# Optimization experiments

Hardware: AMD Instinct MI355X
Metric: run time of the kernel (lower is better)

## Reference

```python
import jax, jax.numpy as jnp
import numpy as np

D_MODEL = 512
PROJ = 2 * D_MODEL  # 1024
N_STATES = 32
KSIZE = 4
LN_EPS = 1e-3  # keras LayerNormalization default epsilon


def setup_inputs() -> dict:
    key = jax.random.key(0)
    ks = jax.random.split(key, 16)
    B, L = 2, 2048
    s_in = 1.0 / np.sqrt(D_MODEL)
    s_pr = 1.0 / np.sqrt(PROJ)
    x = jax.random.normal(ks[0], (B, L, D_MODEL), dtype=jnp.float32)
    # LayerNorm params
    ln_gamma = jnp.ones((D_MODEL,), jnp.float32)
    ln_beta = jnp.zeros((D_MODEL,), jnp.float32)
    # dense1 / dense2: d_model -> proj
    W1 = jax.random.normal(ks[1], (D_MODEL, PROJ), jnp.float32) * s_in
    b1 = jnp.zeros((PROJ,), jnp.float32)
    W2 = jax.random.normal(ks[2], (D_MODEL, PROJ), jnp.float32) * s_in
    b2 = jnp.zeros((PROJ,), jnp.float32)
    # depthwise causal conv1d: kernel (K, 1, PROJ) in WIO layout, groups=PROJ
    conv_k = jax.random.normal(ks[3], (KSIZE, 1, PROJ), jnp.float32) * 0.5
    conv_b = jnp.zeros((PROJ,), jnp.float32)
    # SSM params
    A_log = jnp.log(jnp.broadcast_to(jnp.arange(1, N_STATES + 1, dtype=jnp.float32), (PROJ, N_STATES)))
    D_skip = jnp.ones((PROJ,), jnp.float32)
    WB = jax.random.normal(ks[4], (PROJ, N_STATES), jnp.float32) * s_pr
    bB = jnp.zeros((N_STATES,), jnp.float32)
    WC = jax.random.normal(ks[5], (PROJ, N_STATES), jnp.float32) * s_pr
    bC = jnp.zeros((N_STATES,), jnp.float32)
    Wd = jax.random.normal(ks[6], (PROJ, PROJ), jnp.float32) * s_pr
    bd = jnp.zeros((PROJ,), jnp.float32)
    # dense3: proj -> d_model
    W3 = jax.random.normal(ks[7], (PROJ, D_MODEL), jnp.float32) * s_pr
    b3 = jnp.zeros((D_MODEL,), jnp.float32)
    return dict(x=x, ln_gamma=ln_gamma, ln_beta=ln_beta, W1=W1, b1=b1, W2=W2, b2=b2,
                conv_k=conv_k, conv_b=conv_b, A_log=A_log, D_skip=D_skip,
                WB=WB, bB=bB, WC=WC, bC=bC, Wd=Wd, bd=bd, W3=W3, b3=b3)


def _layernorm(x, gamma, beta):
    mu = jnp.mean(x, axis=-1, keepdims=True)
    var = jnp.mean(jnp.square(x - mu), axis=-1, keepdims=True)
    return (x - mu) * jax.lax.rsqrt(var + LN_EPS) * gamma + beta


def _causal_dwconv(x, k, b):
    # x: [B,L,C], k: [K,1,C], depthwise causal conv (left-pad K-1)
    y = jax.lax.conv_general_dilated(
        x, k, window_strides=(1,), padding=[(KSIZE - 1, 0)],
        dimension_numbers=('NWC', 'WIO', 'NWC'), feature_group_count=PROJ)
    return y + b


def _selective_scan(u, delta, A, Bm, Cm, D_skip):
    # u, delta: [B,L,D]; A: [D,N]; Bm, Cm: [B,L,N]; D_skip: [D]
    deltaA = jnp.einsum('bld,dn->bldn', delta, A)                 # [B,L,D,N]
    deltaBu = jnp.einsum('bld,bld,bln->bldn', delta, u, Bm)        # [B,L,D,N]
    # shift deltaA left by one along L, zero at the end (pad trick in source)
    shifted = jnp.concatenate([deltaA[:, 1:], jnp.zeros_like(deltaA[:, :1])], axis=1)
    # reversed cumsum along L, then exp
    e = jnp.exp(jnp.flip(jnp.cumsum(jnp.flip(shifted, axis=1), axis=1), axis=1))
    xs = jnp.cumsum(deltaBu * e, axis=1) / (e + 1e-12)
    y = jnp.einsum('bldn,bln->bld', xs, Cm)
    return y + u * D_skip


def reference(x, ln_gamma, ln_beta, W1, b1, W2, b2, conv_k, conv_b,
              A_log, D_skip, WB, bB, WC, bC, Wd, bd, W3, b3):
    h = _layernorm(x, ln_gamma, ln_beta)
    x1 = h @ W1 + b1                      # [B,L,PROJ]
    x1 = _causal_dwconv(x1, conv_k, conv_b)
    x1 = jax.nn.silu(x1)
    A = -jnp.exp(A_log)                    # [PROJ,N]
    Cm = x1 @ WC + bC                      # [B,L,N]
    Bm = x1 @ WB + bB                      # [B,L,N]
    delta = jax.nn.softplus(x1 @ Wd + bd)  # [B,L,PROJ]
    y = _selective_scan(x1, delta, A, Bm, Cm, D_skip)
    x2 = jax.nn.silu(h @ W2 + b2)
    out = (y * x2) @ W3 + b3 + x           # residual; dropout is identity at inference
    return out
```

## Files before the change

### kernel.cpp

```cpp
#include <hip/hip_runtime.h>
#include <stdint.h>

#define L_SEQ 2048
#define BATCH 2
#define DMODEL 512
#define PROJ 1024
#define NST 32
#define NCAT 1152
#define ROWS (BATCH*L_SEQ)
#define THRESH 50.0f

typedef float f32x4 __attribute__((ext_vector_type(4)));
typedef short short8 __attribute__((ext_vector_type(8)));

__device__ inline float bf2f(unsigned short u){ uint32_t x=((uint32_t)u)<<16; float f; __builtin_memcpy(&f,&x,4); return f; }
__device__ inline unsigned short f2bf(float f){ uint32_t x; __builtin_memcpy(&x,&f,4); uint32_t r=x+0x7FFFu+((x>>16)&1u); return (unsigned short)(r>>16); }
__device__ inline float siluf(float x){ return x/(1.f+__expf(-x)); }
__device__ inline float softplusf(float x){ return x>20.f? x : log1pf(__expf(x)); }

#define AS1(p) ((const __attribute__((address_space(1))) void*)(p))
#define AS3(p) ((__attribute__((address_space(3))) void*)(p))

template<int N> __device__ inline void wait_vmcnt(){
  if constexpr (N==0)      asm volatile("s_waitcnt vmcnt(0)" ::: "memory");
  else if constexpr (N==4) asm volatile("s_waitcnt vmcnt(4)" ::: "memory");
  else if constexpr (N==8) asm volatile("s_waitcnt vmcnt(8)" ::: "memory");
  else                     asm volatile("s_waitcnt vmcnt(12)" ::: "memory");
}

__global__ __launch_bounds__(256)
void prep_kernel(const float* __restrict__ W1, const float* __restrict__ b1,
                 const float* __restrict__ W2, const float* __restrict__ b2,
                 const float* __restrict__ Wd, const float* __restrict__ bd,
                 const float* __restrict__ WB, const float* __restrict__ bB,
                 const float* __restrict__ WC, const float* __restrict__ bC,
                 const float* __restrict__ W3,
                 unsigned short* __restrict__ W12t, unsigned short* __restrict__ Wcatt,
                 unsigned short* __restrict__ W3t, float* __restrict__ bias12,
                 float* __restrict__ biascat)
{
  __shared__ float tile[32][33];
  int bid = blockIdx.x;
  int lx = threadIdx.x & 31, ly = threadIdx.x >> 5;
  if (bid < 1024) {
    int kt = bid & 15, nt = bid >> 4;
    int k0 = kt*32, n0 = nt*32;
    const float* S = (n0 < 1024) ? W1 : W2;
    int nc = (n0 < 1024) ? n0 : n0 - 1024;
#pragma unroll
    for (int i=0;i<4;i++)
      tile[ly+i*8][lx] = S[(size_t)(k0+ly+i*8)*1024 + nc + lx];
    __syncthreads();
#pragma unroll
    for (int i=0;i<4;i++)
      W12t[(size_t)(n0+ly+i*8)*512 + k0 + lx] = f2bf(tile[lx][ly+i*8]);
    return;
  }
  if (bid < 2176) {
    int t = bid - 1024;
    int kt = t & 31, nt = t >> 5;
    int k0 = kt*32, n0 = nt*32;
#pragma unroll
    for (int i=0;i<4;i++){
      int k = k0 + ly + i*8;
      float v;
      if (n0 < 1024)       v = Wd[(size_t)k*1024 + n0 + lx];
      else if (n0 == 1024) v = WB[(size_t)k*32 + lx];
      else if (n0 == 1056) v = WC[(size_t)k*32 + lx];
      else                 v = 0.f;
      tile[ly+i*8][lx] = v;
    }
    __syncthreads();
#pragma unroll
    for (int i=0;i<4;i++)
      Wcatt[(size_t)(n0+ly+i*8)*1024 + k0 + lx] = f2bf(tile[lx][ly+i*8]);
    return;
  }
  if (bid < 2688) {
    int t = bid - 2176;
    int kt = t & 31, nt = t >> 5;
    int k0 = kt*32, n0 = nt*32;
#pragma unroll
    for (int i=0;i<4;i++)
      tile[ly+i*8][lx] = W3[(size_t)(k0+ly+i*8)*512 + n0 + lx];
    __syncthreads();
#pragma unroll
    for (int i=0;i<4;i++)
      W3t[(size_t)(n0+ly+i*8)*1024 + k0 + lx] = f2bf(tile[lx][ly+i*8]);
    return;
  }
  int j = (bid - 2688)*256 + threadIdx.x;
  if (j < 2048) { bias12[j] = (j < 1024) ? b1[j] : b2[j-1024]; return; }
  j -= 2048;
  if (j < NCAT) biascat[j] = (j < 1024) ? bd[j] : (j < 1056) ? bB[j-1024] : (j < 1088) ? bC[j-1056] : 0.f;
}

__global__ __launch_bounds__(256)
void ln_kernel(const float* __restrict__ x, const float* __restrict__ gamma,
               const float* __restrict__ beta, unsigned short* __restrict__ H)
{
  int row = blockIdx.x*4 + (threadIdx.x >> 6);
  int lane = threadIdx.x & 63;
  const float4* xr = (const float4*)(x + (size_t)row*DMODEL);
  float4 v0 = xr[lane];
  float4 v1 = xr[lane+64];
  float s = v0.x+v0.y+v0.z+v0.w + v1.x+v1.y+v1.z+v1.w;
  float q = v0.x*v0.x+v0.y*v0.y+v0.z*v0.z+v0.w*v0.w
          + v1.x*v1.x+v1.y*v1.y+v1.z*v1.z+v1.w*v1.w;
#pragma unroll
  for (int m=32;m>0;m>>=1){ s += __shfl_xor(s,m); q += __shfl_xor(q,m); }
  float mu = s*(1.f/DMODEL);
  float var = q*(1.f/DMODEL) - mu*mu;
  float rs = rsqrtf(var + 1e-3f);
  int c0 = lane*4, c1 = 256 + lane*4;
  float4 g0 = *(const float4*)&gamma[c0]; float4 g1 = *(const float4*)&gamma[c1];
  float4 t0 = *(const float4*)&beta[c0];  float4 t1 = *(const float4*)&beta[c1];
  ushort4 o0, o1;
  o0.x = f2bf((v0.x-mu)*rs*g0.x + t0.x);
  o0.y = f2bf((v0.y-mu)*rs*g0.y + t0.y);
  o0.z = f2bf((v0.z-mu)*rs*g0.z + t0.z);
  o0.w = f2bf((v0.w-mu)*rs*g0.w + t0.w);
  o1.x = f2bf((v1.x-mu)*rs*g1.x + t1.x);
  o1.y = f2bf((v1.y-mu)*rs*g1.y + t1.y);
  o1.z = f2bf((v1.z-mu)*rs*g1.z + t1.z);
  o1.w = f2bf((v1.w-mu)*rs*g1.w + t1.w);
  *(ushort4*)&H[(size_t)row*DMODEL + c0] = o0;
  *(ushort4*)&H[(size_t)row*DMODEL + c1] = o1;
}

template<int MODE>
__global__ __launch_bounds__(256)
void gemm128(const unsigned short* __restrict__ A, const unsigned short* __restrict__ Bt,
             void* __restrict__ Cv, const float* __restrict__ bias,
             int M, int N, int K)
{
  constexpr int BK = 64;
  constexpr int LPT = 8;
  __shared__ unsigned short As[2][128*BK];
  __shared__ unsigned short Bs[2][128*BK];
  int tid = threadIdx.x;
  int lane = tid & 63, wid = tid >> 6;
  int wm = wid >> 1, wn = wid & 1;

  int gx = gridDim.x;
  int nwg = gx * gridDim.y;
  int L = blockIdx.y*gx + blockIdx.x;
  int W = (L & 7)*(nwg >> 3) + (L >> 3);
  int bx = W % gx, by = W / gx;
  int m0 = bx*128, n0 = by*128;

  f32x4 acc[4][4];
#pragma unroll
  for (int i=0;i<4;i++)
#pragma unroll
    for (int j=0;j<4;j++)
#pragma unroll
      for (int e=0;e<4;e++) acc[i][j][e] = 0.f;

  const unsigned short* ap[4];
  const unsigned short* bp[4];
#pragma unroll
  for (int j=0;j<4;j++){
    int s = tid + j*256;
    int row = s >> 3, kc = ((s & 7) ^ (row & 7)) * 8;
    ap[j] = A + (size_t)(m0+row)*K + kc;
    bp[j] = Bt + (size_t)(n0+row)*K + kc;
  }

  auto stage = [&](int buf){
#pragma unroll
    for (int j=0;j<4;j++){
      __builtin_amdgcn_global_load_lds(AS1(ap[j]), AS3(&As[buf][(size_t)(j*256 + wid*64)*8]), 16, 0, 0);
      ap[j] += BK;
    }
#pragma unroll
    for (int j=0;j<4;j++){
      __builtin_amdgcn_global_load_lds(AS1(bp[j]), AS3(&Bs[buf][(size_t)(j*256 + wid*64)*8]), 16, 0, 0);
      bp[j] += BK;
    }
  };

  stage(0);
  stage(1);
  int T = K/BK;
  int r = lane & 15, kb = lane >> 4;
  for (int t = 0; t < T; ++t) {
    int rb = t & 1;
    if (t+1 < T) wait_vmcnt<LPT>();
    else         wait_vmcnt<0>();
    __builtin_amdgcn_s_barrier();
    short8 af[2][4], bfr[2][4];
#pragma unroll
    for (int ks=0; ks<2; ++ks) {
      int cx = (ks*4 + kb) ^ (r & 7);
#pragma unroll
      for (int i=0;i<4;i++){
        int row = wm*64 + i*16 + r;
        af[ks][i] = *(const short8*)&As[rb][(row*8 + cx)*8];
      }
#pragma unroll
      for (int j=0;j<4;j++){
        int row = wn*64 + j*16 + r;
        bfr[ks][j] = *(const short8*)&Bs[rb][(row*8 + cx)*8];
      }
    }
    asm volatile("s_waitcnt lgkmcnt(0)" ::: "memory");
    __builtin_amdgcn_sched_barrier(0);
    __builtin_amdgcn_s_barrier();
    if (t+2 < T) stage(rb);
    __builtin_amdgcn_s_setprio(1);
#pragma unroll
    for (int ks=0; ks<2; ++ks)
#pragma unroll
      for (int i=0;i<4;i++)
#pragma unroll
        for (int j=0;j<4;j++)
          acc[i][j] = __builtin_amdgcn_mfma_f32_16x16x32_bf16(af[ks][i], bfr[ks][j], acc[i][j], 0,0,0);
    __builtin_amdgcn_s_setprio(0);
  }

  int rr = (lane >> 4)*4, cc = lane & 15;
#pragma unroll
  for (int i=0;i<4;i++)
#pragma unroll
    for (int j=0;j<4;j++) {
      int col = n0 + wn*64 + j*16 + cc;
      float bcol = (MODE == 1) ? bias[col] : 0.f;
#pragma unroll
      for (int e=0;e<4;e++) {
        int row = m0 + wm*64 + i*16 + rr + e;
        float v = acc[i][j][e];
        if constexpr (MODE == 2) {
          v += bias[row];
          if (row < 1024) v = softplusf(v);
          ((float*)Cv)[(size_t)row*N + col] = v;
        } else {
          ((unsigned short*)Cv)[(size_t)row*N + col] = f2bf(v + bcol);
        }
      }
    }
}

__global__ __launch_bounds__(256)
void gemm64s(const unsigned short* __restrict__ A, const unsigned short* __restrict__ Bt,
             float* __restrict__ Pp, int M, int N, int K, int Kfull)
{
  constexpr int BK = 64;
  constexpr int LPT = 4;
  __shared__ unsigned short As[3][64*BK];
  __shared__ unsigned short Bs[3][64*BK];
  int tid = threadIdx.x;
  int lane = tid & 63, wid = tid >> 6;
  int wm = wid >> 1, wn = wid & 1;
  int gx = gridDim.x;
  int nwg = gx * gridDim.y;
  int L = blockIdx.y*gx + blockIdx.x;
  int W = (L & 7)*(nwg >> 3) + (L >> 3);
  int bx = W % gx, by = W / gx;
  int m0 = bx*64, n0 = by*64;
  int kofs = blockIdx.z*K;

  f32x4 acc[2][2];
#pragma unroll
  for (int i=0;i<2;i++)
#pragma unroll
    for (int j=0;j<2;j++)
#pragma unroll
      for (int e=0;e<4;e++) acc[i][j][e] = 0.f;

  const unsigned short* ap[2];
  const unsigned short* bp[2];
#pragma unroll
  for (int j=0;j<2;j++){
    int s = tid + j*256;
    int row = s >> 3, kc = ((s & 7) ^ (row & 7)) * 8;
    ap[j] = A + (size_t)(m0+row)*Kfull + kofs + kc;
    bp[j] = Bt + (size_t)(n0+row)*Kfull + kofs + kc;
  }
  auto stage = [&](int buf){
#pragma unroll
    for (int j=0;j<2;j++){
      __builtin_amdgcn_global_load_lds(AS1(ap[j]), AS3(&As[buf][(size_t)(j*256 + wid*64)*8]), 16, 0, 0);
      ap[j] += BK;
    }
#pragma unroll
    for (int j=0;j<2;j++){
      __builtin_amdgcn_global_load_lds(AS1(bp[j]), AS3(&Bs[buf][(size_t)(j*256 + wid*64)*8]), 16, 0, 0);
      bp[j] += BK;
    }
  };
  stage(0); stage(1);
  int T = K/BK;
  int rb = 0, wb = 2;
  int r = lane & 15, kb = lane >> 4;
  for (int t = 0; t < T; ++t) {
    if (t+1 < T) wait_vmcnt<LPT>();
    else         wait_vmcnt<0>();
    __builtin_amdgcn_s_barrier();
    if (t+2 < T) { stage(wb); wb = (wb==2)?0:wb+1; }
#pragma unroll
    for (int ks=0; ks<2; ++ks) {
      int cx = (ks*4 + kb) ^ (r & 7);
      short8 af[2], bfr[2];
#pragma unroll
      for (int i=0;i<2;i++) af[i]  = *(const short8*)&As[rb][((wm*32 + i*16 + r)*8 + cx)*8];
#pragma unroll
      for (int j=0;j<2;j++) bfr[j] = *(const short8*)&Bs[rb][((wn*32 + j*16 + r)*8 + cx)*8];
      __builtin_amdgcn_s_setprio(1);
#pragma unroll
      for (int i=0;i<2;i++)
#pragma unroll
        for (int j=0;j<2;j++)
          acc[i][j] = __builtin_amdgcn_mfma_f32_16x16x32_bf16(af[i], bfr[j], acc[i][j], 0,0,0);
      __builtin_amdgcn_s_setprio(0);
    }
    rb = (rb==2)?0:rb+1;
  }
  int rr = (lane >> 4)*4, cc = lane & 15;
#pragma unroll
  for (int i=0;i<2;i++)
#pragma unroll
    for (int j=0;j<2;j++) {
      int col = n0 + wn*32 + j*16 + cc;
#pragma unroll
      for (int e=0;e<4;e++) {
        int row = m0 + wm*32 + i*16 + rr + e;
        Pp[(size_t)blockIdx.z*M*N + (size_t)row*N + col] = acc[i][j][e];
      }
    }
}

__global__ __launch_bounds__(256)
void reduce_kernel(const float* __restrict__ P, const float* __restrict__ x,
                   const float* __restrict__ b3, float* __restrict__ out)
{
  size_t i = ((size_t)blockIdx.x*256 + threadIdx.x)*4;
  int col = (int)(i & 511);
  float4 a = *(const float4*)&P[i];
  float4 b = *(const float4*)&P[(size_t)ROWS*512 + i];
  float4 xv = *(const float4*)&x[i];
  float4 bv = *(const float4*)&b3[col];
  float4 o;
  o.x = a.x + b.x + xv.x + bv.x;
  o.y = a.y + b.y + xv.y + bv.y;
  o.z = a.z + b.z + xv.z + bv.z;
  o.w = a.w + b.w + xv.w + bv.w;
  *(float4*)&out[i] = o;
}

__global__ __launch_bounds__(256)
void conv_silu_kernel(const unsigned short* __restrict__ P12, const float* __restrict__ ck,
                      const float* __restrict__ cb, unsigned short* __restrict__ ubf,
                      unsigned short* __restrict__ x2bf)
{
  int gid = blockIdx.x*256 + threadIdx.x;
  int c4 = gid & 511;
  int row = gid >> 9;
  int l = row & (L_SEQ-1);
  if (c4 < 256) {
    int c = c4*4;
    float4 bv = *(const float4*)&cb[c];
    float r0=bv.x, r1=bv.y, r2=bv.z, r3=bv.w;
#pragma unroll
    for (int t=0;t<4;t++){
      int lsrc = l - 3 + t;
      if (lsrc >= 0) {
        ushort4 xv = *(const ushort4*)&P12[(size_t)(row-3+t)*2048 + c];
        float4 kv = *(const float4*)&ck[t*PROJ + c];
        r0 = fmaf(bf2f(xv.x),kv.x,r0);
        r1 = fmaf(bf2f(xv.y),kv.y,r1);
        r2 = fmaf(bf2f(xv.z),kv.z,r2);
        r3 = fmaf(bf2f(xv.w),kv.w,r3);
      }
    }
    ushort4 o;
    o.x=f2bf(siluf(r0)); o.y=f2bf(siluf(r1)); o.z=f2bf(siluf(r2)); o.w=f2bf(siluf(r3));
    *(ushort4*)&ubf[(size_t)row*PROJ + c] = o;
  } else {
    int c = (c4-256)*4;
    ushort4 xv = *(const ushort4*)&P12[(size_t)row*2048 + 1024 + c];
    ushort4 o;
    o.x=f2bf(siluf(bf2f(xv.x))); o.y=f2bf(siluf(bf2f(xv.y)));
    o.z=f2bf(siluf(bf2f(xv.z))); o.w=f2bf(siluf(bf2f(xv.w)));
    *(ushort4*)&x2bf[(size_t)row*PROJ + c] = o;
  }
}

__global__ __launch_bounds__(256)
void sscan_kernel(const float* __restrict__ CT, const unsigned short* __restrict__ ubf,
                  const float* __restrict__ A_log, int* __restrict__ l0out,
                  unsigned short* __restrict__ ystate)
{
  __shared__ float suf8sh[8][256];
  int tid = threadIdx.x;
  int n = tid & 31, gsub = tid >> 5;
  int G = blockIdx.x*8 + gsub;
  int b = G >> 10, d = G & 1023;
  const float* dT = CT + (size_t)d*ROWS + b*L_SEQ;

  float mysum = 0.f;
  {
    const float4* c4 = (const float4*)(dT + n*64);
    for (int it=0; it<16; ++it){ float4 v = c4[it]; mysum += v.x+v.y+v.z+v.w; }
  }
  float incl = mysum;
#pragma unroll
  for (int dlt=1; dlt<32; dlt<<=1){ float t = __shfl_up(incl, dlt, 32); if (n >= dlt) incl += t; }
  float Tot = __shfl(incl, 31, 32);
  float excl = incl - mysum;
  int cnt = 0;
  {
    const float4* c4 = (const float4*)(dT + n*64);
    float run = excl;
    for (int it=0; it<16; ++it){
      float4 v = c4[it];
      if ((it & 1) == 0) suf8sh[gsub][n*8 + (it>>1)] = Tot - run;
      cnt += (Tot - run >= THRESH); run += v.x;
      cnt += (Tot - run >= THRESH); run += v.y;
      cnt += (Tot - run >= THRESH); run += v.z;
      cnt += (Tot - run >= THRESH); run += v.w;
    }
  }
#pragma unroll
  for (int m=16;m>0;m>>=1) cnt += __shfl_xor(cnt, m, 32);
  int myl0 = cnt > 0 ? cnt-1 : 0;
  if (n == 0) l0out[G] = myl0;
  __syncthreads();

  int base = min(myl0, __shfl_xor(myl0, 32)) & ~7;
  float np1 = __expf(A_log[d*NST + n]);
  const float* Br = CT + (size_t)(1024+n)*ROWS + b*L_SEQ;
  const float* Cr = CT + (size_t)(1056+n)*ROWS + b*L_SEQ;
  const unsigned short* ub = ubf + (size_t)b*L_SEQ*PROJ + d;
  unsigned short* yb = ystate + (size_t)b*L_SEQ*PROJ + d;
  float s = 0.f;
  for (int l = base; l < L_SEQ; l += 8) {
    float4 d0 = *(const float4*)&dT[l];
    float4 d1 = *(const float4*)&dT[l+4];
    float4 B0 = *(const float4*)&Br[l];
    float4 B1 = *(const float4*)&Br[l+4];
    float4 C0 = *(const float4*)&Cr[l];
    float4 C1 = *(const float4*)&Cr[l+4];
    float sufv = suf8sh[gsub][l >> 3];
    float dl[8] = {d0.x,d0.y,d0.z,d0.w,d1.x,d1.y,d1.z,d1.w};
    float Bv[8] = {B0.x,B0.y,B0.z,B0.w,B1.x,B1.y,B1.z,B1.w};
    float Cv[8] = {C0.x,C0.y,C0.z,C0.w,C1.x,C1.y,C1.z,C1.w};
    float uu[8];
#pragma unroll
    for (int t=0;t<8;t++) uu[t] = bf2f(ub[(size_t)(l+t)*PROJ]);
    float cum = 0.f;
#pragma unroll
    for (int t=0;t<8;t++){
      cum += dl[t];
      float decay = __expf(-dl[t]*np1);
      s = fmaf(decay, s, dl[t]*uu[t]*Bv[t]);
      float gte = 1.f/(1.f + 1e-12f*__expf(np1*(sufv - cum)));
      float contrib = s*gte*Cv[t];
#pragma unroll
      for (int m=16;m>0;m>>=1) contrib += __shfl_xor(contrib, m);
      if (n == 0) yb[(size_t)(l+t)*PROJ] = f2bf(contrib);
    }
  }
}

__global__ __launch_bounds__(256)
void zmul_kernel(const unsigned short* __restrict__ ystate, const unsigned short* __restrict__ ubf,
                 const unsigned short* __restrict__ x2bf, const float* __restrict__ Dskip,
                 const int* __restrict__ l0arr, unsigned short* __restrict__ zbf)
{
  size_t i = ((size_t)blockIdx.x*256 + threadIdx.x)*4;
  int d = (int)(i & (PROJ-1));
  int row = (int)(i >> 10);
  int l = row & (L_SEQ-1);
  int b = row >> 11;
  int4 l0v = *(const int4*)&l0arr[b*PROJ + d];
  ushort4 yu = *(const ushort4*)&ystate[i];
  float ysx = (l >= l0v.x) ? bf2f(yu.x) : 0.f;
  float ysy = (l >= l0v.y) ? bf2f(yu.y) : 0.f;
  float ysz = (l >= l0v.z) ? bf2f(yu.z) : 0.f;
  float ysw = (l >= l0v.w) ? bf2f(yu.w) : 0.f;
  ushort4 uu = *(const ushort4*)&ubf[i];
  ushort4 xx = *(const ushort4*)&x2bf[i];
  float4 Dv = *(const float4*)&Dskip[d];
  ushort4 o;
  o.x = f2bf((ysx + bf2f(uu.x)*Dv.x)*bf2f(xx.x));
  o.y = f2bf((ysy + bf2f(uu.y)*Dv.y)*bf2f(xx.y));
  o.z = f2bf((ysz + bf2f(uu.z)*Dv.z)*bf2f(xx.z));
  o.w = f2bf((ysw + bf2f(uu.w)*Dv.w)*bf2f(xx.w));
  *(ushort4*)&zbf[i] = o;
}

extern "C" void kernel_launch(void* const* d_in, const int* in_sizes, int n_in,
                              void* d_out, int out_size, void* d_ws, size_t ws_size,
                              hipStream_t stream)
{
  const float* x     = (const float*)d_in[0];
  const float* ln_g  = (const float*)d_in[1];
  const float* ln_b  = (const float*)d_in[2];
  const float* W1    = (const float*)d_in[3];
  const float* b1    = (const float*)d_in[4];
  const float* W2    = (const float*)d_in[5];
  const float* b2    = (const float*)d_in[6];
  const float* convk = (const float*)d_in[7];
  const float* convb = (const float*)d_in[8];
  const float* A_log = (const float*)d_in[9];
  const float* Dskip = (const float*)d_in[10];
  const float* WB    = (const float*)d_in[11];
  const float* bB    = (const float*)d_in[12];
  const float* WC    = (const float*)d_in[13];
  const float* bC    = (const float*)d_in[14];
  const float* Wd    = (const float*)d_in[15];
  const float* bd    = (const float*)d_in[16];
  const float* W3    = (const float*)d_in[17];
  const float* b3    = (const float*)d_in[18];

  char* w = (char*)d_ws;
  auto alloc = [&](size_t bytes){ char* p = w; w += (bytes + 255) & ~(size_t)255; return p; };
  unsigned short* Hbf    = (unsigned short*)alloc((size_t)ROWS*DMODEL*2);
  unsigned short* W12t   = (unsigned short*)alloc((size_t)2048*512*2);
  unsigned short* Wcatt  = (unsigned short*)alloc((size_t)NCAT*1024*2);
  unsigned short* W3t    = (unsigned short*)alloc((size_t)512*1024*2);
  float*          bias12 = (float*)alloc(2048*4);
  float*          biascat= (float*)alloc(NCAT*4);
  unsigned short* P12    = (unsigned short*)alloc((size_t)ROWS*2048*2);
  unsigned short* ubf    = (unsigned short*)alloc((size_t)ROWS*PROJ*2);
  unsigned short* x2bf   = (unsigned short*)alloc((size_t)ROWS*PROJ*2);
  float*          CT     = (float*)alloc((size_t)NCAT*ROWS*4);
  int*            l0arr  = (int*)alloc(2048*4);
  unsigned short* ystate = (unsigned short*)alloc((size_t)ROWS*PROJ*2);
  unsigned short* zbf    = (unsigned short*)alloc((size_t)ROWS*PROJ*2);
  float*          Pp     = (float*)alloc((size_t)2*ROWS*512*4);

  prep_kernel<<<2701, 256, 0, stream>>>(W1,b1,W2,b2,Wd,bd,WB,bB,WC,bC,W3,
                                        W12t,Wcatt,W3t,bias12,biascat);
  ln_kernel<<<ROWS/4, 256, 0, stream>>>(x, ln_g, ln_b, Hbf);

  dim3 g1(ROWS/128, 2048/128);
  gemm128<1><<<g1, 256, 0, stream>>>(Hbf, W12t, P12, bias12, ROWS, 2048, DMODEL);

  conv_silu_kernel<<<ROWS*512/256, 256, 0, stream>>>(P12, convk, convb, ubf, x2bf);

  dim3 g2(NCAT/128, ROWS/128);
  gemm128<2><<<g2, 256, 0, stream>>>(Wcatt, ubf, CT, biascat, NCAT, ROWS, PROJ);

  sscan_kernel<<<2048/8, 256, 0, stream>>>(CT, ubf, A_log, l0arr, ystate);

  zmul_kernel<<<(ROWS*PROJ/4)/256, 256, 0, stream>>>(ystate, ubf, x2bf, Dskip, l0arr, zbf);

  dim3 g3(ROWS/64, 512/64, 2);
  gemm64s<<<g3, 256, 0, stream>>>(zbf, W3t, Pp, ROWS, 512, 512, PROJ);
  reduce_kernel<<<(ROWS*512/4)/256, 256, 0, stream>>>(Pp, x, b3, (float*)d_out);
}
```

Measured before the change: 159.8 us.

## Fuse LN into prep, silu x2 into GEMM epilogue, zmul into scan

Merges weight prep and layernorm into one launch and applies silu for x2 directly in the first GEMM epilogue, so conv only handles the u half. It drops the padded 1152 concat to 1088 columns and moves that GEMM to 64-wide tiles. The scan now writes the final z = (y + u*D)*x2 itself, with a pre-pass filling u*D*x2 for positions before each channel's start index. This removes the ystate and l0 buffers and the separate zmul pass. The cost is extra per-element work inside the serial scan and a smaller-tile GEMM that may reuse data less.

```diff
diff --git a/kernel.cpp b/kernel.cpp
--- a/kernel.cpp
+++ b/kernel.cpp
@@ -6,7 +6,7 @@
 #define DMODEL 512
 #define PROJ 1024
 #define NST 32
-#define NCAT 1152
+#define NCATU 1088
 #define ROWS (BATCH*L_SEQ)
 #define THRESH 50.0f
 
@@ -29,15 +29,17 @@
 }
 
 __global__ __launch_bounds__(256)
-void prep_kernel(const float* __restrict__ W1, const float* __restrict__ b1,
-                 const float* __restrict__ W2, const float* __restrict__ b2,
-                 const float* __restrict__ Wd, const float* __restrict__ bd,
-                 const float* __restrict__ WB, const float* __restrict__ bB,
-                 const float* __restrict__ WC, const float* __restrict__ bC,
-                 const float* __restrict__ W3,
-                 unsigned short* __restrict__ W12t, unsigned short* __restrict__ Wcatt,
-                 unsigned short* __restrict__ W3t, float* __restrict__ bias12,
-                 float* __restrict__ biascat)
+void prep_ln_kernel(const float* __restrict__ W1, const float* __restrict__ b1,
+                    const float* __restrict__ W2, const float* __restrict__ b2,
+                    const float* __restrict__ Wd, const float* __restrict__ bd,
+                    const float* __restrict__ WB, const float* __restrict__ bB,
+                    const float* __restrict__ WC, const float* __restrict__ bC,
+                    const float* __restrict__ W3,
+                    unsigned short* __restrict__ W12t, unsigned short* __restrict__ Wcatt,
+                    unsigned short* __restrict__ W3t, float* __restrict__ bias12,
+                    float* __restrict__ biascat,
+                    const float* __restrict__ x, const float* __restrict__ ln_g,
+                    const float* __restrict__ ln_b, unsigned short* __restrict__ H)
 {
   __shared__ float tile[32][33];
   int bid = blockIdx.x;
@@ -56,7 +58,7 @@
       W12t[(size_t)(n0+ly+i*8)*512 + k0 + lx] = f2bf(tile[lx][ly+i*8]);
     return;
   }
-  if (bid < 2176) {
+  if (bid < 2112) {
     int t = bid - 1024;
     int kt = t & 31, nt = t >> 5;
     int k0 = kt*32, n0 = nt*32;
@@ -66,8 +68,7 @@
       float v;
       if (n0 < 1024)       v = Wd[(size_t)k*1024 + n0 + lx];
       else if (n0 == 1024) v = WB[(size_t)k*32 + lx];
-      else if (n0 == 1056) v = WC[(size_t)k*32 + lx];
-      else                 v = 0.f;
+      else                 v = WC[(size_t)k*32 + lx];
       tile[ly+i*8][lx] = v;
     }
     __syncthreads();
@@ -76,8 +77,8 @@
       Wcatt[(size_t)(n0+ly+i*8)*1024 + k0 + lx] = f2bf(tile[lx][ly+i*8]);
     return;
   }
-  if (bid < 2688) {
-    int t = bid - 2176;
+  if (bid < 2624) {
+    int t = bid - 2112;
     int kt = t & 31, nt = t >> 5;
     int k0 = kt*32, n0 = nt*32;
 #pragma unroll
@@ -89,17 +90,14 @@
       W3t[(size_t)(n0+ly+i*8)*1024 + k0 + lx] = f2bf(tile[lx][ly+i*8]);
     return;
   }
-  int j = (bid - 2688)*256 + threadIdx.x;
-  if (j < 2048) { bias12[j] = (j < 1024) ? b1[j] : b2[j-1024]; return; }
-  j -= 2048;
-  if (j < NCAT) biascat[j] = (j < 1024) ? bd[j] : (j < 1056) ? bB[j-1024] : (j < 1088) ? bC[j-1056] : 0.f;
-}
-
-__global__ __launch_bounds__(256)
-void ln_kernel(const float* __restrict__ x, const float* __restrict__ gamma,
-               const float* __restrict__ beta, unsigned short* __restrict__ H)
-{
-  int row = blockIdx.x*4 + (threadIdx.x >> 6);
+  if (bid < 2637) {
+    int j = (bid - 2624)*256 + threadIdx.x;
+    if (j < 2048) { bias12[j] = (j < 1024) ? b1[j] : b2[j-1024]; return; }
+    j -= 2048;
+    if (j < NCATU) biascat[j] = (j < 1024) ? bd[j] : (j < 1056) ? bB[j-1024] : bC[j-1056];
+    return;
+  }
+  int row = (bid - 2637)*4 + (threadIdx.x >> 6);
   int lane = threadIdx.x & 63;
   const float4* xr = (const float4*)(x + (size_t)row*DMODEL);
   float4 v0 = xr[lane];
@@ -113,8 +111,8 @@
   float var = q*(1.f/DMODEL) - mu*mu;
   float rs = rsqrtf(var + 1e-3f);
   int c0 = lane*4, c1 = 256 + lane*4;
-  float4 g0 = *(const float4*)&gamma[c0]; float4 g1 = *(const float4*)&gamma[c1];
-  float4 t0 = *(const float4*)&beta[c0];  float4 t1 = *(const float4*)&beta[c1];
+  float4 g0 = *(const float4*)&ln_g[c0]; float4 g1 = *(const float4*)&ln_g[c1];
+  float4 t0 = *(const float4*)&ln_b[c0]; float4 t1 = *(const float4*)&ln_b[c1];
   ushort4 o0, o1;
   o0.x = f2bf((v0.x-mu)*rs*g0.x + t0.x);
   o0.y = f2bf((v0.y-mu)*rs*g0.y + t0.y);
@@ -128,11 +126,10 @@
   *(ushort4*)&H[(size_t)row*DMODEL + c1] = o1;
 }
 
-template<int MODE>
-__global__ __launch_bounds__(256)
-void gemm128(const unsigned short* __restrict__ A, const unsigned short* __restrict__ Bt,
-             void* __restrict__ Cv, const float* __restrict__ bias,
-             int M, int N, int K)
+__global__ __launch_bounds__(256)
+void gemm128_g1(const unsigned short* __restrict__ A, const unsigned short* __restrict__ Bt,
+                unsigned short* __restrict__ P12n, unsigned short* __restrict__ x2bf,
+                const float* __restrict__ bias, int M, int N, int K)
 {
   constexpr int BK = 64;
   constexpr int LPT = 8;
@@ -141,7 +138,6 @@
   int tid = threadIdx.x;
   int lane = tid & 63, wid = tid >> 6;
   int wm = wid >> 1, wn = wid & 1;
-
   int gx = gridDim.x;
   int nwg = gx * gridDim.y;
   int L = blockIdx.y*gx + blockIdx.x;
@@ -166,7 +162,6 @@
     ap[j] = A + (size_t)(m0+row)*K + kc;
     bp[j] = Bt + (size_t)(n0+row)*K + kc;
   }
-
   auto stage = [&](int buf){
 #pragma unroll
     for (int j=0;j<4;j++){
@@ -179,7 +174,6 @@
       bp[j] += BK;
     }
   };
-
   stage(0);
   stage(1);
   int T = K/BK;
@@ -194,15 +188,9 @@
     for (int ks=0; ks<2; ++ks) {
       int cx = (ks*4 + kb) ^ (r & 7);
 #pragma unroll
-      for (int i=0;i<4;i++){
-        int row = wm*64 + i*16 + r;
-        af[ks][i] = *(const short8*)&As[rb][(row*8 + cx)*8];
-      }
-#pragma unroll
-      for (int j=0;j<4;j++){
-        int row = wn*64 + j*16 + r;
-        bfr[ks][j] = *(const short8*)&Bs[rb][(row*8 + cx)*8];
-      }
+      for (int i=0;i<4;i++) af[ks][i]  = *(const short8*)&As[rb][((wm*64 + i*16 + r)*8 + cx)*8];
+#pragma unroll
+      for (int j=0;j<4;j++) bfr[ks][j] = *(const short8*)&Bs[rb][((wn*64 + j*16 + r)*8 + cx)*8];
     }
     asm volatile("s_waitcnt lgkmcnt(0)" ::: "memory");
     __builtin_amdgcn_sched_barrier(0);
@@ -225,25 +213,22 @@
 #pragma unroll
     for (int j=0;j<4;j++) {
       int col = n0 + wn*64 + j*16 + cc;
-      float bcol = (MODE == 1) ? bias[col] : 0.f;
+      float bcol = bias[col];
 #pragma unroll
       for (int e=0;e<4;e++) {
         int row = m0 + wm*64 + i*16 + rr + e;
-        float v = acc[i][j][e];
-        if constexpr (MODE == 2) {
-          v += bias[row];
-          if (row < 1024) v = softplusf(v);
-          ((float*)Cv)[(size_t)row*N + col] = v;
-        } else {
-          ((unsigned short*)Cv)[(size_t)row*N + col] = f2bf(v + bcol);
-        }
+        float v = acc[i][j][e] + bcol;
+        if (col < 1024) P12n[(size_t)row*1024 + col] = f2bf(v);
+        else            x2bf[(size_t)row*1024 + col - 1024] = f2bf(siluf(v));
       }
     }
 }
 
-__global__ __launch_bounds__(256)
-void gemm64s(const unsigned short* __restrict__ A, const unsigned short* __restrict__ Bt,
-             float* __restrict__ Pp, int M, int N, int K, int Kfull)
+template<int MODE>
+__global__ __launch_bounds__(256)
+void gemm64(const unsigned short* __restrict__ A, const unsigned short* __restrict__ Bt,
+            void* __restrict__ Cv, const float* __restrict__ bias,
+            int M, int N, int K, int Kfull)
 {
   constexpr int BK = 64;
   constexpr int LPT = 4;
@@ -325,7 +310,14 @@
 #pragma unroll
       for (int e=0;e<4;e++) {
         int row = m0 + wm*32 + i*16 + rr + e;
-        Pp[(size_t)blockIdx.z*M*N + (size_t)row*N + col] = acc[i][j][e];
+        float v = acc[i][j][e];
+        if constexpr (MODE == 2) {
+          v += bias[row];
+          if (row < 1024) v = softplusf(v);
+          ((float*)Cv)[(size_t)row*N + col] = v;
+        } else {
+          ((float*)Cv)[(size_t)blockIdx.z*M*N + (size_t)row*N + col] = v;
+        }
       }
     }
 }
@@ -349,47 +341,53 @@
 }
 
 __global__ __launch_bounds__(256)
-void conv_silu_kernel(const unsigned short* __restrict__ P12, const float* __restrict__ ck,
-                      const float* __restrict__ cb, unsigned short* __restrict__ ubf,
-                      unsigned short* __restrict__ x2bf)
+void conv_silu_kernel(const unsigned short* __restrict__ P12n, const float* __restrict__ ck,
+                      const float* __restrict__ cb, unsigned short* __restrict__ ubf)
 {
   int gid = blockIdx.x*256 + threadIdx.x;
-  int c4 = gid & 511;
-  int row = gid >> 9;
+  int c = (gid & 255)*4;
+  int row = gid >> 8;
   int l = row & (L_SEQ-1);
-  if (c4 < 256) {
-    int c = c4*4;
-    float4 bv = *(const float4*)&cb[c];
-    float r0=bv.x, r1=bv.y, r2=bv.z, r3=bv.w;
-#pragma unroll
-    for (int t=0;t<4;t++){
-      int lsrc = l - 3 + t;
-      if (lsrc >= 0) {
-        ushort4 xv = *(const ushort4*)&P12[(size_t)(row-3+t)*2048 + c];
-        float4 kv = *(const float4*)&ck[t*PROJ + c];
-        r0 = fmaf(bf2f(xv.x),kv.x,r0);
-        r1 = fmaf(bf2f(xv.y),kv.y,r1);
-        r2 = fmaf(bf2f(xv.z),kv.z,r2);
-        r3 = fmaf(bf2f(xv.w),kv.w,r3);
-      }
-    }
-    ushort4 o;
-    o.x=f2bf(siluf(r0)); o.y=f2bf(siluf(r1)); o.z=f2bf(siluf(r2)); o.w=f2bf(siluf(r3));
-    *(ushort4*)&ubf[(size_t)row*PROJ + c] = o;
-  } else {
-    int c = (c4-256)*4;
-    ushort4 xv = *(const ushort4*)&P12[(size_t)row*2048 + 1024 + c];
-    ushort4 o;
-    o.x=f2bf(siluf(bf2f(xv.x))); o.y=f2bf(siluf(bf2f(xv.y)));
-    o.z=f2bf(siluf(bf2f(xv.z))); o.w=f2bf(siluf(bf2f(xv.w)));
-    *(ushort4*)&x2bf[(size_t)row*PROJ + c] = o;
-  }
+  float4 bv = *(const float4*)&cb[c];
+  float r0=bv.x, r1=bv.y, r2=bv.z, r3=bv.w;
+#pragma unroll
+  for (int t=0;t<4;t++){
+    int lsrc = l - 3 + t;
+    if (lsrc >= 0) {
+      ushort4 xv = *(const ushort4*)&P12n[(size_t)(row-3+t)*1024 + c];
+      float4 kv = *(const float4*)&ck[t*PROJ + c];
+      r0 = fmaf(bf2f(xv.x),kv.x,r0);
+      r1 = fmaf(bf2f(xv.y),kv.y,r1);
+      r2 = fmaf(bf2f(xv.z),kv.z,r2);
+      r3 = fmaf(bf2f(xv.w),kv.w,r3);
+    }
+  }
+  ushort4 o;
+  o.x=f2bf(siluf(r0)); o.y=f2bf(siluf(r1)); o.z=f2bf(siluf(r2)); o.w=f2bf(siluf(r3));
+  *(ushort4*)&ubf[(size_t)row*PROJ + c] = o;
+}
+
+__global__ __launch_bounds__(256)
+void zmul_pre_kernel(const unsigned short* __restrict__ ubf, const unsigned short* __restrict__ x2bf,
+                     const float* __restrict__ Dskip, unsigned short* __restrict__ zbf)
+{
+  size_t i = ((size_t)blockIdx.x*256 + threadIdx.x)*4;
+  int d = (int)(i & (PROJ-1));
+  ushort4 uu = *(const ushort4*)&ubf[i];
+  ushort4 xx = *(const ushort4*)&x2bf[i];
+  float4 Dv = *(const float4*)&Dskip[d];
+  ushort4 o;
+  o.x = f2bf(bf2f(uu.x)*Dv.x*bf2f(xx.x));
+  o.y = f2bf(bf2f(uu.y)*Dv.y*bf2f(xx.y));
+  o.z = f2bf(bf2f(uu.z)*Dv.z*bf2f(xx.z));
+  o.w = f2bf(bf2f(uu.w)*Dv.w*bf2f(xx.w));
+  *(ushort4*)&zbf[i] = o;
 }
 
 __global__ __launch_bounds__(256)
 void sscan_kernel(const float* __restrict__ CT, const unsigned short* __restrict__ ubf,
-                  const float* __restrict__ A_log, int* __restrict__ l0out,
-                  unsigned short* __restrict__ ystate)
+                  const unsigned short* __restrict__ x2bf, const float* __restrict__ Dskip,
+                  const float* __restrict__ A_log, unsigned short* __restrict__ zbf)
 {
   __shared__ float suf8sh[8][256];
   int tid = threadIdx.x;
@@ -424,15 +422,16 @@
 #pragma unroll
   for (int m=16;m>0;m>>=1) cnt += __shfl_xor(cnt, m, 32);
   int myl0 = cnt > 0 ? cnt-1 : 0;
-  if (n == 0) l0out[G] = myl0;
   __syncthreads();
 
   int base = min(myl0, __shfl_xor(myl0, 32)) & ~7;
   float np1 = __expf(A_log[d*NST + n]);
+  float Ds = Dskip[d];
   const float* Br = CT + (size_t)(1024+n)*ROWS + b*L_SEQ;
   const float* Cr = CT + (size_t)(1056+n)*ROWS + b*L_SEQ;
   const unsigned short* ub = ubf + (size_t)b*L_SEQ*PROJ + d;
-  unsigned short* yb = ystate + (size_t)b*L_SEQ*PROJ + d;
+  const unsigned short* xb = x2bf + (size_t)b*L_SEQ*PROJ + d;
+  unsigned short* zb = zbf + (size_t)b*L_SEQ*PROJ + d;
   float s = 0.f;
   for (int l = base; l < L_SEQ; l += 8) {
     float4 d0 = *(const float4*)&dT[l];
@@ -458,36 +457,12 @@
       float contrib = s*gte*Cv[t];
 #pragma unroll
       for (int m=16;m>0;m>>=1) contrib += __shfl_xor(contrib, m);
-      if (n == 0) yb[(size_t)(l+t)*PROJ] = f2bf(contrib);
-    }
-  }
-}
-
-__global__ __launch_bounds__(256)
-void zmul_kernel(const unsigned short* __restrict__ ystate, const unsigned short* __restrict__ ubf,
-                 const unsigned short* __restrict__ x2bf, const float* __restrict__ Dskip,
-                 const int* __restrict__ l0arr, unsigned short* __restrict__ zbf)
-{
-  size_t i = ((size_t)blockIdx.x*256 + threadIdx.x)*4;
-  int d = (int)(i & (PROJ-1));
-  int row = (int)(i >> 10);
-  int l = row & (L_SEQ-1);
-  int b = row >> 11;
-  int4 l0v = *(const int4*)&l0arr[b*PROJ + d];
-  ushort4 yu = *(const ushort4*)&ystate[i];
-  float ysx = (l >= l0v.x) ? bf2f(yu.x) : 0.f;
-  float ysy = (l >= l0v.y) ? bf2f(yu.y) : 0.f;
-  float ysz = (l >= l0v.z) ? bf2f(yu.z) : 0.f;
-  float ysw = (l >= l0v.w) ? bf2f(yu.w) : 0.f;
-  ushort4 uu = *(const ushort4*)&ubf[i];
-  ushort4 xx = *(const ushort4*)&x2bf[i];
-  float4 Dv = *(const float4*)&Dskip[d];
-  ushort4 o;
-  o.x = f2bf((ysx + bf2f(uu.x)*Dv.x)*bf2f(xx.x));
-  o.y = f2bf((ysy + bf2f(uu.y)*Dv.y)*bf2f(xx.y));
-  o.z = f2bf((ysz + bf2f(uu.z)*Dv.z)*bf2f(xx.z));
-  o.w = f2bf((ysw + bf2f(uu.w)*Dv.w)*bf2f(xx.w));
-  *(ushort4*)&zbf[i] = o;
+      if (n == 0) {
+        float x2v = bf2f(xb[(size_t)(l+t)*PROJ]);
+        zb[(size_t)(l+t)*PROJ] = f2bf((contrib + uu[t]*Ds)*x2v);
+      }
+    }
+  }
 }
 
 extern "C" void kernel_launch(void* const* d_in, const int* in_sizes, int n_in,
@@ -518,36 +493,34 @@
   auto alloc = [&](size_t bytes){ char* p = w; w += (bytes + 255) & ~(size_t)255; return p; };
   unsigned short* Hbf    = (unsigned short*)alloc((size_t)ROWS*DMODEL*2);
   unsigned short* W12t   = (unsigned short*)alloc((size_t)2048*512*2);
-  unsigned short* Wcatt  = (unsigned short*)alloc((size_t)NCAT*1024*2);
+  unsigned short* Wcatt  = (unsigned short*)alloc((size_t)NCATU*1024*2);
   unsigned short* W3t    = (unsigned short*)alloc((size_t)512*1024*2);
   float*          bias12 = (float*)alloc(2048*4);
-  float*          biascat= (float*)alloc(NCAT*4);
-  unsigned short* P12    = (unsigned short*)alloc((size_t)ROWS*2048*2);
+  float*          biascat= (float*)alloc(NCATU*4);
+  unsigned short* P12n   = (unsigned short*)alloc((size_t)ROWS*1024*2);
   unsigned short* ubf    = (unsigned short*)alloc((size_t)ROWS*PROJ*2);
   unsigned short* x2bf   = (unsigned short*)alloc((size_t)ROWS*PROJ*2);
-  float*          CT     = (float*)alloc((size_t)NCAT*ROWS*4);
-  int*            l0arr  = (int*)alloc(2048*4);
-  unsigned short* ystate = (unsigned short*)alloc((size_t)ROWS*PROJ*2);
+  float*          CT     = (float*)alloc((size_t)NCATU*ROWS*4);
   unsigned short* zbf    = (unsigned short*)alloc((size_t)ROWS*PROJ*2);
   float*          Pp     = (float*)alloc((size_t)2*ROWS*512*4);
 
-  prep_kernel<<<2701, 256, 0, stream>>>(W1,b1,W2,b2,Wd,bd,WB,bB,WC,bC,W3,
-                                        W12t,Wcatt,W3t,bias12,biascat);
-  ln_kernel<<<ROWS/4, 256, 0, stream>>>(x, ln_g, ln_b, Hbf);
+  prep_ln_kernel<<<3661, 256, 0, stream>>>(W1,b1,W2,b2,Wd,bd,WB,bB,WC,bC,W3,
+                                           W12t,Wcatt,W3t,bias12,biascat,
+                                           x, ln_g, ln_b, Hbf);
 
   dim3 g1(ROWS/128, 2048/128);
-  gemm128<1><<<g1, 256, 0, stream>>>(Hbf, W12t, P12, bias12, ROWS, 2048, DMODEL);
-
-  conv_silu_kernel<<<ROWS*512/256, 256, 0, stream>>>(P12, convk, convb, ubf, x2bf);
-
-  dim3 g2(NCAT/128, ROWS/128);
-  gemm128<2><<<g2, 256, 0, stream>>>(Wcatt, ubf, CT, biascat, NCAT, ROWS, PROJ);
-
-  sscan_kernel<<<2048/8, 256, 0, stream>>>(CT, ubf, A_log, l0arr, ystate);
-
-  zmul_kernel<<<(ROWS*PROJ/4)/256, 256, 0, stream>>>(ystate, ubf, x2bf, Dskip, l0arr, zbf);
+  gemm128_g1<<<g1, 256, 0, stream>>>(Hbf, W12t, P12n, x2bf, bias12, ROWS, 2048, DMODEL);
+
+  conv_silu_kernel<<<ROWS*256/256, 256, 0, stream>>>(P12n, convk, convb, ubf);
+
+  zmul_pre_kernel<<<(ROWS*PROJ/4)/256, 256, 0, stream>>>(ubf, x2bf, Dskip, zbf);
+
+  dim3 g2(NCATU/64, ROWS/64);
+  gemm64<2><<<g2, 256, 0, stream>>>(Wcatt, ubf, CT, biascat, NCATU, ROWS, PROJ, PROJ);
+
+  sscan_kernel<<<2048/8, 256, 0, stream>>>(CT, ubf, x2bf, Dskip, A_log, zbf);
 
   dim3 g3(ROWS/64, 512/64, 2);
-  gemm64s<<<g3, 256, 0, stream>>>(zbf, W3t, Pp, ROWS, 512, 512, PROJ);
+  gemm64<5><<<g3, 256, 0, stream>>>(zbf, W3t, Pp, b3, ROWS, 512, 512, PROJ);
   reduce_kernel<<<(ROWS*512/4)/256, 256, 0, stream>>>(Pp, x, b3, (float*)d_out);
 }
```

New measurement: 162.9 us. About the same (+1.9%).
